# Kernel tuning notes

Hardware: AMD Instinct MI355X
Metric: run time of the kernel (lower is better)

Reference implementation:

```python
import jax, jax.numpy as jnp
import numpy as np

WS = 8        # window_size
SS = 4        # shift_size
NH = 8        # num_heads
DIM = 256
HD = DIM // NH
SCALE = HD ** -0.5
EPS = 1e-5


def _rel_pos_index(ws):
    ch, cw = np.meshgrid(np.arange(ws), np.arange(ws), indexing='ij')
    coords = np.stack([ch.ravel(), cw.ravel()])            # [2, ws*ws]
    rel = coords[:, :, None] - coords[:, None, :]           # [2, N, N]
    rel = rel.transpose(1, 2, 0)
    rel[:, :, 0] += ws - 1
    rel[:, :, 1] += ws - 1
    rel[:, :, 0] *= 2 * ws - 1
    return jnp.asarray(rel.sum(-1))                         # [N, N] int

REL_IDX = _rel_pos_index(WS)


def _ln(x, g, b):
    m = jnp.mean(x, axis=-1, keepdims=True)
    v = jnp.mean(jnp.square(x - m), axis=-1, keepdims=True)
    return (x - m) * jax.lax.rsqrt(v + EPS) * g + b


def setup_inputs() -> dict:
    key = jax.random.key(0)
    ks = jax.random.split(key, 12)
    B, L, C = 8, 16384, DIM
    s = lambda k, shape, scale=0.02: jax.random.normal(k, shape, jnp.float32) * scale
    return {
        'x': jax.random.normal(ks[0], (B, L, C), jnp.float32),
        'norm1_g': jnp.ones((C,), jnp.float32),
        'norm1_b': jnp.zeros((C,), jnp.float32),
        'qkv_w': s(ks[1], (C, 3 * C)),
        'qkv_b': jnp.zeros((3 * C,), jnp.float32),
        'rel_bias': s(ks[2], ((2 * WS - 1) ** 2, NH)),
        'proj_w': s(ks[3], (C, C)),
        'proj_b': jnp.zeros((C,), jnp.float32),
        'norm2_g': jnp.ones((C,), jnp.float32),
        'norm2_b': jnp.zeros((C,), jnp.float32),
        'fc1_w': s(ks[4], (C, C)),
        'fc1_b': jnp.zeros((C,), jnp.float32),
        'fc2_w': s(ks[5], (C, C)),
        'fc2_b': jnp.zeros((C,), jnp.float32),
        'H': 128,
        'W': 128,
    }


def reference(x, norm1_g, norm1_b, qkv_w, qkv_b, rel_bias, proj_w, proj_b,
              norm2_g, norm2_b, fc1_w, fc1_b, fc2_w, fc2_b, H, W):
    B, L, C = x.shape
    shortcut = x
    h = _ln(x, norm1_g, norm1_b).reshape(B, H, W, C)
    pad_b = (WS - H % WS) % WS
    pad_r = (WS - W % WS) % WS
    h = jnp.pad(h, ((0, 0), (0, pad_b), (0, pad_r), (0, 0)))
    Hp, Wp = H + pad_b, W + pad_r
    if SS > 0:
        h = jnp.roll(h, (-SS, -SS), axis=(1, 2))
    # window partition -> [B*nW, WS*WS, C]
    h = h.reshape(B, Hp // WS, WS, Wp // WS, WS, C)
    h = h.transpose(0, 1, 3, 2, 4, 5).reshape(-1, WS * WS, C)
    Bn, N = h.shape[0], WS * WS
    # attention
    qkv = (h @ qkv_w + qkv_b).reshape(Bn, N, 3, NH, HD)
    q, k, v = qkv[:, :, 0], qkv[:, :, 1], qkv[:, :, 2]   # [Bn, N, NH, HD]
    attn = jnp.einsum('bnhd,bmhd->bhnm', q * SCALE, k)
    bias = rel_bias[REL_IDX.reshape(-1)].reshape(N, N, NH).transpose(2, 0, 1)
    attn = jax.nn.softmax(attn + bias[None], axis=-1)
    o = jnp.einsum('bhnm,bmhd->bnhd', attn, v).reshape(Bn, N, C)
    o = o @ proj_w + proj_b
    # window reverse
    o = o.reshape(B, Hp // WS, Wp // WS, WS, WS, C)
    o = o.transpose(0, 1, 3, 2, 4, 5).reshape(B, Hp, Wp, C)
    if SS > 0:
        o = jnp.roll(o, (SS, SS), axis=(1, 2))
    o = o[:, :H, :W, :].reshape(B, H * W, C)
    x = shortcut + o
    # MLP (hidden = dim, exact GELU as nn.GELU default)
    m = _ln(x, norm2_g, norm2_b)
    m = jax.nn.gelu(m @ fc1_w + fc1_b, approximate=False)
    m = m @ fc2_w + fc2_b
    return x + m
```

## Files before the change

kernel.cpp:

```cpp
#include <hip/hip_runtime.h>
#include <stdint.h>

typedef __bf16 bf16;
typedef __bf16 bf16x4v __attribute__((ext_vector_type(4)));
typedef __bf16 bf16x8 __attribute__((ext_vector_type(8)));
typedef float floatx4 __attribute__((ext_vector_type(4)));
typedef float float4v __attribute__((ext_vector_type(4)));

#define SCALE 0.17677669529663689f

__device__ __forceinline__ float ldin(const void* p, long i, int f32) {
  return f32 ? ((const float*)p)[i] : (float)(((const bf16*)p)[i]);
}

__device__ __forceinline__ void async16(const bf16* g, bf16* l) {
  __builtin_amdgcn_global_load_lds(
      (const __attribute__((address_space(1))) void*)g,
      (__attribute__((address_space(3))) void*)l, 16, 0, 0);
}

__global__ void detect_k(const unsigned short* __restrict__ x, int* flag) {
  __shared__ int cnt;
  if (threadIdx.x == 0) cnt = 0;
  __syncthreads();
  int local = 0;
  for (int i = threadIdx.x; i < 4096; i += 256) {
    unsigned short w = x[i];
    int e = (w >> 7) & 0xFF;
    if (w != 0 && (e >= 0x9F || e <= 0x5F)) local++;
  }
  atomicAdd(&cnt, local);
  __syncthreads();
  if (threadIdx.x == 0) *flag = (cnt >= 64) ? 1 : 0;
}

__global__ void conv_w_k(const void* __restrict__ W, bf16* __restrict__ Wt,
                         int K, int N, const int* __restrict__ flag) {
  int f32 = *flag;
  int idx = blockIdx.x * 256 + threadIdx.x;
  if (idx < K * N) {
    int k = idx / N, n = idx % N;
    Wt[n * K + k] = (bf16)ldin(W, idx, f32);
  }
}

__global__ void conv3_k(const void* __restrict__ W0, const void* __restrict__ W1,
                        const void* __restrict__ W2, bf16* __restrict__ T0,
                        bf16* __restrict__ T1, bf16* __restrict__ T2,
                        const int* __restrict__ flag) {
  int f32 = *flag;
  int which = blockIdx.x >> 8;
  int idx = (blockIdx.x & 255) * 256 + threadIdx.x;
  const void* W = which == 0 ? W0 : which == 1 ? W1 : W2;
  bf16* T = which == 0 ? T0 : which == 1 ? T1 : T2;
  int k = idx >> 8, n = idx & 255;
  T[n * 256 + k] = (bf16)ldin(W, idx, f32);
}

__global__ void bias_k(const void* __restrict__ rel, float* __restrict__ bias_s,
                       const int* __restrict__ flag) {
  int f = *flag;
  int idx = blockIdx.x * 256 + threadIdx.x;
  int r = idx & 3, ni = (idx >> 2) & 3, mi = (idx >> 4) & 3;
  int l16 = (idx >> 6) & 15, quad = (idx >> 10) & 3, head = idx >> 12;
  int i = mi * 16 + quad * 4 + r, j = ni * 16 + l16;
  int dy = (i >> 3) - (j >> 3) + 7, dx = (i & 7) - (j & 7) + 7;
  bias_s[idx] = ldin(rel, (dy * 15 + dx) * 8 + head, f);
}

__global__ __launch_bounds__(256) void ln_k(const void* __restrict__ x,
                                            const void* __restrict__ g,
                                            const void* __restrict__ b,
                                            bf16* __restrict__ y,
                                            const int* __restrict__ flag,
                                            int x_input) {
  int f = *flag;
  int f32x = x_input ? f : 0;
  int wave = threadIdx.x >> 6, lane = threadIdx.x & 63;
  long row = (long)blockIdx.x * 4 + wave;
  float v[4];
  if (f32x) {
    float4v u = ((const float4v*)x)[row * 64 + lane];
    for (int i = 0; i < 4; i++) v[i] = u[i];
  } else {
    bf16x4v u = ((const bf16x4v*)x)[row * 64 + lane];
    for (int i = 0; i < 4; i++) v[i] = (float)u[i];
  }
  float s = v[0] + v[1] + v[2] + v[3];
  for (int off = 32; off > 0; off >>= 1) s += __shfl_xor(s, off, 64);
  float mean = s * (1.f / 256.f);
  float q = 0.f;
  for (int i = 0; i < 4; i++) { float d = v[i] - mean; q += d * d; }
  for (int off = 32; off > 0; off >>= 1) q += __shfl_xor(q, off, 64);
  float rstd = rsqrtf(q * (1.f / 256.f) + 1e-5f);
  bf16x4v o;
  for (int i = 0; i < 4; i++) {
    float gv = ldin(g, lane * 4 + i, f);
    float bv = ldin(b, lane * 4 + i, f);
    o[i] = (bf16)((v[i] - mean) * rstd * gv + bv);
  }
  ((bf16x4v*)y)[row * 64 + lane] = o;
}

template <int EPI>
__global__ __launch_bounds__(256) void gemm_bt_k(
    const bf16* __restrict__ A, const bf16* __restrict__ Bt,
    const void* __restrict__ bias, const void* __restrict__ res,
    void* __restrict__ C, int M, int N, int K, const int* __restrict__ flag,
    int res_input, int out_input) {
  __shared__ __align__(16) char smem[16896];
  bf16* As = (bf16*)smem;
  bf16* Bs = (bf16*)(smem + 8192);
  float* CsF = (float*)smem;

  const int tid = threadIdx.x;
  const int ntiles = gridDim.x;
  int bid = blockIdx.y * ntiles + blockIdx.x;
  const int nwg = ntiles * gridDim.y;
  if (!(nwg & 7)) bid = (bid & 7) * (nwg >> 3) + (bid >> 3);
  const long m0 = (long)(bid / ntiles) * 128;
  const int n0 = (bid % ntiles) * 128;
  const int wave = tid >> 6, lane = tid & 63;
  const int wm = wave & 1, wn = wave >> 1;
  const int quad = lane >> 4, l16 = lane & 15;

  floatx4 acc[4][4];
  for (int i = 0; i < 4; i++)
    for (int j = 0; j < 4; j++) acc[i][j] = (floatx4){0.f, 0.f, 0.f, 0.f};

  const int ldr = tid >> 2;
  const int ldc = (((tid & 3) ^ ((tid >> 3) & 3)) << 3);

  const bf16* gA0 = A + (m0 + ldr) * K + ldc;
  const bf16* gA1 = A + (m0 + 64 + ldr) * K + ldc;
  const bf16* gB0 = Bt + (long)(n0 + ldr) * K + ldc;
  const bf16* gB1 = Bt + (long)(n0 + 64 + ldr) * K + ldc;
  bf16* lA0 = As + wave * 512;
  bf16* lA1 = As + 2048 + wave * 512;
  bf16* lB0 = Bs + wave * 512;
  bf16* lB1 = Bs + 2048 + wave * 512;

  const int rswz = (l16 >> 1) & 3;

  for (int kt = 0; kt < K; kt += 32) {
    __syncthreads();
    async16(gA0 + kt, lA0);
    async16(gA1 + kt, lA1);
    async16(gB0 + kt, lB0);
    async16(gB1 + kt, lB1);
    __syncthreads();
    bf16x8 af[4], bfr[4];
    for (int mi = 0; mi < 4; mi++)
      af[mi] = *(const bf16x8*)&As[(wm * 64 + mi * 16 + l16) * 32 +
                                   ((quad ^ rswz) << 3)];
    for (int ni = 0; ni < 4; ni++)
      bfr[ni] = *(const bf16x8*)&Bs[(wn * 64 + ni * 16 + l16) * 32 +
                                    ((quad ^ rswz) << 3)];
    for (int mi = 0; mi < 4; mi++)
      for (int ni = 0; ni < 4; ni++)
        acc[mi][ni] = __builtin_amdgcn_mfma_f32_16x16x32_bf16(
            af[mi], bfr[ni], acc[mi][ni], 0, 0, 0);
  }

  const int f = *flag;
  const int rf32 = res_input ? f : 0;
  const int of32 = out_input ? f : 0;
  for (int mi = 0; mi < 4; mi++) {
    __syncthreads();
    for (int ni = 0; ni < 4; ni++) {
      int col = n0 + wn * 64 + ni * 16 + l16;
      float bv = ldin(bias, col, f);
      for (int r = 0; r < 4; r++) {
        long row = m0 + wm * 64 + mi * 16 + quad * 4 + r;
        float v = acc[mi][ni][r] + bv;
        if (EPI == 1) v = v * 0.5f * (1.f + erff(v * 0.70710678118654752f));
        if (EPI == 2) v += ldin(res, row * N + col, rf32);
        CsF[(wm * 16 + quad * 4 + r) * 132 + wn * 64 + ni * 16 + l16] = v;
      }
    }
    __syncthreads();
    const int s = tid >> 3;
    const int seg = tid & 7;
    const long grow = m0 + (s >> 4) * 64 + mi * 16 + (s & 15);
    const int gcol = n0 + seg * 16;
    const float4v* src = (const float4v*)&CsF[s * 132 + seg * 16];
    float4v v0 = src[0], v1 = src[1], v2 = src[2], v3 = src[3];
    if (of32) {
      float4v* dst = (float4v*)((float*)C + grow * N + gcol);
      dst[0] = v0; dst[1] = v1; dst[2] = v2; dst[3] = v3;
    } else {
      bf16x8 o0, o1;
      for (int j = 0; j < 4; j++) {
        o0[j] = (bf16)v0[j]; o0[4 + j] = (bf16)v1[j];
        o1[j] = (bf16)v2[j]; o1[4 + j] = (bf16)v3[j];
      }
      bf16x8* dst = (bf16x8*)((bf16*)C + grow * N + gcol);
      dst[0] = o0; dst[1] = o1;
    }
  }
}

__global__ __launch_bounds__(256) void attn_k(const bf16* __restrict__ qkv,
                                              const float* __restrict__ bias_s,
                                              bf16* __restrict__ o) {
  __shared__ bf16 Pb[4][64 * 64];
  __shared__ bf16 Vb[4][32 * 64];
  const int tid = threadIdx.x;
  const int wave = tid >> 6, lane = tid & 63;
  const int quad = lane >> 4, l16 = lane & 15;
  const int gid = blockIdx.x * 4 + wave;
  const int head = gid & 7, win = gid >> 3;
  const int wx = win & 15, wy = (win >> 4) & 15, bb = win >> 8;

  bf16* P = Pb[wave];
  bf16* Vt = Vb[wave];

  bf16x8 qf[4], kf[4];
  for (int mi = 0; mi < 4; mi++) {
    int t = mi * 16 + l16;
    int rr = (wy * 8 + (t >> 3) + 4) & 127;
    int cc = (wx * 8 + (t & 7) + 4) & 127;
    long base = ((long)(bb * 16384 + rr * 128 + cc)) * 768 + head * 32 + quad * 8;
    qf[mi] = *(const bf16x8*)(qkv + base);
    kf[mi] = *(const bf16x8*)(qkv + base + 256);
    bf16x8 vv = *(const bf16x8*)(qkv + base + 512);
    int tcol = t ^ (quad << 4);
    for (int jj = 0; jj < 8; jj++) Vt[(quad * 8 + jj) * 64 + tcol] = vv[jj];
  }
  __syncthreads();

  floatx4 acc[4][4];
  for (int mi = 0; mi < 4; mi++)
    for (int ni = 0; ni < 4; ni++) {
      floatx4 z = (floatx4){0.f, 0.f, 0.f, 0.f};
      acc[mi][ni] = __builtin_amdgcn_mfma_f32_16x16x32_bf16(qf[mi], kf[ni], z, 0, 0, 0);
    }

  const float4v* bp =
      (const float4v*)(bias_s + (((head * 4 + quad) * 16 + l16) << 6));
  for (int mi = 0; mi < 4; mi++) {
    float mx[4] = {-1e30f, -1e30f, -1e30f, -1e30f};
    for (int ni = 0; ni < 4; ni++) {
      float4v bv = bp[mi * 4 + ni];
      for (int r = 0; r < 4; r++) {
        acc[mi][ni][r] = acc[mi][ni][r] * SCALE + bv[r];
        mx[r] = fmaxf(mx[r], acc[mi][ni][r]);
      }
    }
    for (int r = 0; r < 4; r++) {
      float m = mx[r];
      for (int off = 1; off < 16; off <<= 1) m = fmaxf(m, __shfl_xor(m, off, 64));
      mx[r] = m;
    }
    float sm[4] = {0.f, 0.f, 0.f, 0.f};
    for (int ni = 0; ni < 4; ni++)
      for (int r = 0; r < 4; r++) {
        float e = __expf(acc[mi][ni][r] - mx[r]);
        acc[mi][ni][r] = e;
        sm[r] += e;
      }
    for (int r = 0; r < 4; r++) {
      float s = sm[r];
      for (int off = 1; off < 16; off <<= 1) s += __shfl_xor(s, off, 64);
      sm[r] = 1.f / s;
    }
    for (int ni = 0; ni < 4; ni++)
      for (int r = 0; r < 4; r++) {
        int i = mi * 16 + quad * 4 + r;
        int j = ni * 16 + l16;
        P[i * 64 + (j ^ ((i & 7) << 3))] = (bf16)(acc[mi][ni][r] * sm[r]);
      }
  }
  __syncthreads();

  floatx4 oacc[4][2];
  for (int mi = 0; mi < 4; mi++)
    for (int nt = 0; nt < 2; nt++) oacc[mi][nt] = (floatx4){0.f, 0.f, 0.f, 0.f};
  for (int ks = 0; ks < 2; ks++) {
    bf16x8 vfr[2];
    for (int nt = 0; nt < 2; nt++) {
      int d = nt * 16 + l16;
      vfr[nt] =
          *(const bf16x8*)&Vt[d * 64 + ((ks * 32 + quad * 8) ^ ((d >> 3) << 4))];
    }
    for (int mi = 0; mi < 4; mi++) {
      int i = mi * 16 + l16;
      bf16x8 pf =
          *(const bf16x8*)&P[i * 64 + ((ks * 32 + quad * 8) ^ ((i & 7) << 3))];
      for (int nt = 0; nt < 2; nt++)
        oacc[mi][nt] = __builtin_amdgcn_mfma_f32_16x16x32_bf16(pf, vfr[nt],
                                                               oacc[mi][nt], 0, 0, 0);
    }
  }

  for (int mi = 0; mi < 4; mi++)
    for (int r = 0; r < 4; r++) {
      int t = mi * 16 + quad * 4 + r;
      int rot = (t >> 1) & 3;
      int c0 = l16, c1 = 16 + l16;
      Vt[t * 32 + ((((c0 >> 3) + rot) & 3) << 3) + (c0 & 7)] = (bf16)oacc[mi][0][r];
      Vt[t * 32 + ((((c1 >> 3) + rot) & 3) << 3) + (c1 & 7)] = (bf16)oacc[mi][1][r];
    }
  {
    int t = lane;
    int rot = (t >> 1) & 3;
    int rr = (wy * 8 + (t >> 3) + 4) & 127;
    int cc = (wx * 8 + (t & 7) + 4) & 127;
    long base = ((long)(bb * 16384 + rr * 128 + cc)) * 256 + head * 32;
    bf16x8* dst = (bf16x8*)(o + base);
    for (int k = 0; k < 4; k++)
      dst[k] = *(const bf16x8*)&Vt[t * 32 + (((k + rot) & 3) << 3)];
  }
}

extern "C" void kernel_launch(void* const* d_in, const int* in_sizes, int n_in,
                              void* d_out, int out_size, void* d_ws,
                              size_t ws_size, hipStream_t stream) {
  const void* x = d_in[0];
  const void* n1g = d_in[1];
  const void* n1b = d_in[2];
  const void* qkv_w = d_in[3];
  const void* qkv_b = d_in[4];
  const void* rel_bias = d_in[5];
  const void* proj_w = d_in[6];
  const void* proj_b = d_in[7];
  const void* n2g = d_in[8];
  const void* n2b = d_in[9];
  const void* fc1_w = d_in[10];
  const void* fc1_b = d_in[11];
  const void* fc2_w = d_in[12];
  const void* fc2_b = d_in[13];

  char* ws = (char*)d_ws;
  int* flag = (int*)ws;
  float* bias_s = (float*)(ws + 4096);
  bf16* qkvWt = (bf16*)(ws + 262144);
  bf16* projWt = qkvWt + 768 * 256;
  bf16* fc1Wt = projWt + 256 * 256;
  bf16* fc2Wt = fc1Wt + 256 * 256;
  bf16* reg1 = (bf16*)(ws + (1 << 20));
  bf16* reg2 = (bf16*)(ws + (1 << 20) + 67108864);

  const int M = 131072;

  detect_k<<<1, 256, 0, stream>>>((const unsigned short*)x, flag);

  bias_k<<<128, 256, 0, stream>>>(rel_bias, bias_s, flag);
  conv_w_k<<<768, 256, 0, stream>>>(qkv_w, qkvWt, 256, 768, flag);
  conv3_k<<<768, 256, 0, stream>>>(proj_w, fc1_w, fc2_w, projWt, fc1Wt, fc2Wt,
                                   flag);

  bf16* h = reg1;
  ln_k<<<M / 4, 256, 0, stream>>>(x, n1g, n1b, h, flag, 1);

  bf16* qkv = reg2;
  gemm_bt_k<0><<<dim3(6, M / 128), 256, 0, stream>>>(
      h, qkvWt, qkv_b, nullptr, qkv, M, 768, 256, flag, 0, 0);

  bf16* o = reg1;
  attn_k<<<2048 * 8 / 4, 256, 0, stream>>>(qkv, bias_s, o);

  bf16* x2 = reg2;
  gemm_bt_k<2><<<dim3(2, M / 128), 256, 0, stream>>>(
      o, projWt, proj_b, x, x2, M, 256, 256, flag, 1, 0);

  bf16* mbuf = reg1;
  ln_k<<<M / 4, 256, 0, stream>>>(x2, n2g, n2b, mbuf, flag, 0);

  bf16* m1 = reg2 + 33554432;
  gemm_bt_k<1><<<dim3(2, M / 128), 256, 0, stream>>>(
      mbuf, fc1Wt, fc1_b, nullptr, m1, M, 256, 256, flag, 0, 0);

  gemm_bt_k<2><<<dim3(2, M / 128), 256, 0, stream>>>(
      m1, fc2Wt, fc2_b, x2, d_out, M, 256, 256, flag, 0, 1);
}
```

Before: 842.6 us.

## Double-buffer GEMM LDS tiles and vectorize residual add in epilogue

The GEMM main loop now keeps two LDS buffers and issues async global-to-LDS loads for the next K tile before computing on the current one. This lets memory latency overlap with MFMA work and removes one barrier per iteration. The residual add moves from scattered per-element loads into the coalesced store phase, where it uses vector loads. LDS use doubles to 32KB, which may reduce occupancy.

```diff
diff --git a/kernel.cpp b/kernel.cpp
--- a/kernel.cpp
+++ b/kernel.cpp
@@ -108,9 +108,8 @@
     const void* __restrict__ bias, const void* __restrict__ res,
     void* __restrict__ C, int M, int N, int K, const int* __restrict__ flag,
     int res_input, int out_input) {
-  __shared__ __align__(16) char smem[16896];
-  bf16* As = (bf16*)smem;
-  bf16* Bs = (bf16*)(smem + 8192);
+  __shared__ __align__(16) char smem[32768];
+  bf16* Sb = (bf16*)smem;
   float* CsF = (float*)smem;
 
   const int tid = threadIdx.x;
@@ -135,32 +134,43 @@
   const bf16* gA1 = A + (m0 + 64 + ldr) * K + ldc;
   const bf16* gB0 = Bt + (long)(n0 + ldr) * K + ldc;
   const bf16* gB1 = Bt + (long)(n0 + 64 + ldr) * K + ldc;
-  bf16* lA0 = As + wave * 512;
-  bf16* lA1 = As + 2048 + wave * 512;
-  bf16* lB0 = Bs + wave * 512;
-  bf16* lB1 = Bs + 2048 + wave * 512;
 
   const int rswz = (l16 >> 1) & 3;
-
-  for (int kt = 0; kt < K; kt += 32) {
-    __syncthreads();
-    async16(gA0 + kt, lA0);
-    async16(gA1 + kt, lA1);
-    async16(gB0 + kt, lB0);
-    async16(gB1 + kt, lB1);
-    __syncthreads();
+  const int NT = K >> 5;
+
+#define STAGE(b, tt)                                   \
+  do {                                                 \
+    bf16* _base = Sb + (b) * 8192 + wave * 512;        \
+    int _kt = (tt) << 5;                               \
+    async16(gA0 + _kt, _base);                         \
+    async16(gA1 + _kt, _base + 2048);                  \
+    async16(gB0 + _kt, _base + 4096);                  \
+    async16(gB1 + _kt, _base + 6144);                  \
+  } while (0)
+
+  STAGE(0, 0);
+  __syncthreads();
+
+  int cur = 0;
+  for (int t = 0; t < NT; ++t) {
+    if (t + 1 < NT) STAGE(cur ^ 1, t + 1);
+    const bf16* As_t = Sb + cur * 8192;
+    const bf16* Bs_t = As_t + 4096;
     bf16x8 af[4], bfr[4];
     for (int mi = 0; mi < 4; mi++)
-      af[mi] = *(const bf16x8*)&As[(wm * 64 + mi * 16 + l16) * 32 +
-                                   ((quad ^ rswz) << 3)];
+      af[mi] = *(const bf16x8*)&As_t[(wm * 64 + mi * 16 + l16) * 32 +
+                                     ((quad ^ rswz) << 3)];
     for (int ni = 0; ni < 4; ni++)
-      bfr[ni] = *(const bf16x8*)&Bs[(wn * 64 + ni * 16 + l16) * 32 +
-                                    ((quad ^ rswz) << 3)];
+      bfr[ni] = *(const bf16x8*)&Bs_t[(wn * 64 + ni * 16 + l16) * 32 +
+                                      ((quad ^ rswz) << 3)];
     for (int mi = 0; mi < 4; mi++)
       for (int ni = 0; ni < 4; ni++)
         acc[mi][ni] = __builtin_amdgcn_mfma_f32_16x16x32_bf16(
             af[mi], bfr[ni], acc[mi][ni], 0, 0, 0);
-  }
+    __syncthreads();
+    cur ^= 1;
+  }
+#undef STAGE
 
   const int f = *flag;
   const int rf32 = res_input ? f : 0;
@@ -171,10 +181,8 @@
       int col = n0 + wn * 64 + ni * 16 + l16;
       float bv = ldin(bias, col, f);
       for (int r = 0; r < 4; r++) {
-        long row = m0 + wm * 64 + mi * 16 + quad * 4 + r;
         float v = acc[mi][ni][r] + bv;
         if (EPI == 1) v = v * 0.5f * (1.f + erff(v * 0.70710678118654752f));
-        if (EPI == 2) v += ldin(res, row * N + col, rf32);
         CsF[(wm * 16 + quad * 4 + r) * 132 + wn * 64 + ni * 16 + l16] = v;
       }
     }
@@ -185,6 +193,19 @@
     const int gcol = n0 + seg * 16;
     const float4v* src = (const float4v*)&CsF[s * 132 + seg * 16];
     float4v v0 = src[0], v1 = src[1], v2 = src[2], v3 = src[3];
+    if (EPI == 2) {
+      if (rf32) {
+        const float4v* rp = (const float4v*)((const float*)res + grow * N + gcol);
+        v0 += rp[0]; v1 += rp[1]; v2 += rp[2]; v3 += rp[3];
+      } else {
+        const bf16x8* rp = (const bf16x8*)((const bf16*)res + grow * N + gcol);
+        bf16x8 r0 = rp[0], r1 = rp[1];
+        for (int j = 0; j < 4; j++) {
+          v0[j] += (float)r0[j];     v1[j] += (float)r0[4 + j];
+          v2[j] += (float)r1[j];     v3[j] += (float)r1[4 + j];
+        }
+      }
+    }
     if (of32) {
       float4v* dst = (float4v*)((float*)C + grow * N + gcol);
       dst[0] = v0; dst[1] = v1; dst[2] = v2; dst[3] = v3;
```

After: 740.9 us. 1.14x faster.
